# Kernel optimization log

Measured on AMD Instinct MI355X. Metric: run time of the kernel, lower is better.

## Reference

```python
import jax, jax.numpy as jnp
import numpy as np

N_NODES = 50000
N_EDGES = 1600000
N_GRAPHS = 512
IN_DIM = 64
HID = 128
OUT_DIM = 10


def setup_inputs() -> dict:
    key = jax.random.key(0)
    ks = jax.random.split(key, 12)
    x = jax.random.normal(ks[0], (N_NODES, IN_DIM), dtype=jnp.float32)
    edge_index = jax.random.randint(ks[1], (2, N_EDGES), 0, N_NODES, dtype=jnp.int64)
    batch = jnp.sort(jax.random.randint(ks[2], (N_NODES,), 0, N_GRAPHS, dtype=jnp.int64))
    edge_attr = jax.random.uniform(ks[3], (N_EDGES,), dtype=jnp.float32)
    # glorot-ish init for weights
    def lin(k, fan_in, fan_out):
        s = (6.0 / (fan_in + fan_out)) ** 0.5
        return jax.random.uniform(k, (fan_in, fan_out), minval=-s, maxval=s, dtype=jnp.float32)
    return {
        "x": x, "edge_index": edge_index, "batch": batch, "edge_attr": edge_attr,
        "W1": lin(ks[4], IN_DIM, HID), "b1": jnp.zeros((HID,), jnp.float32),
        "W2": lin(ks[5], HID, HID), "b2": jnp.zeros((HID,), jnp.float32),
        "Wm1": lin(ks[6], HID, HID), "bm1": jnp.zeros((HID,), jnp.float32),
        "Wm2": lin(ks[7], HID, OUT_DIM), "bm2": jnp.zeros((OUT_DIM,), jnp.float32),
    }


def _gcn_conv(x, edge_index, edge_weight, W, b, num_nodes):
    """PyG GCNConv: add self-loops, symmetric norm with edge weights, x@W, scatter-add, +bias."""
    loop = jnp.arange(num_nodes, dtype=edge_index.dtype)
    src = jnp.concatenate([edge_index[0], loop])
    dst = jnp.concatenate([edge_index[1], loop])
    ew = jnp.concatenate([edge_weight, jnp.ones((num_nodes,), edge_weight.dtype)])
    deg = jax.ops.segment_sum(ew, dst, num_segments=num_nodes)  # [N]
    dinv = jnp.where(deg > 0, jax.lax.rsqrt(jnp.where(deg > 0, deg, 1.0)), 0.0)
    norm = dinv[src] * ew * dinv[dst]  # [E+N]
    h = x @ W  # [N, F_out]
    msg = h[src] * norm[:, None]  # gather + scale
    out = jax.ops.segment_sum(msg, dst, num_segments=num_nodes)
    return out + b


def reference(x, edge_index, batch, edge_attr, W1, b1, W2, b2, Wm1, bm1, Wm2, bm2):
    n = x.shape[0]
    h = _gcn_conv(x, edge_index, edge_attr, W1, b1, n)
    h = jax.nn.relu(h)  # dropout = identity in eval mode
    h = _gcn_conv(h, edge_index, edge_attr, W2, b2, n)
    h = jax.nn.relu(h)
    pooled = jax.ops.segment_sum(h, batch, num_segments=N_GRAPHS)  # global_add_pool
    z = jax.nn.relu(pooled @ Wm1 + bm1)
    return z @ Wm2 + bm2  # [num_graphs, out_dim]
```

## Files before the change

kernel.cpp:

```cpp
#include <hip/hip_runtime.h>
#include <hip/hip_bf16.h>
#include <hip/hip_fp16.h>
#include <cstdint>

#define HIDC 128
#define FIXSCALE 4194304.0f
#define FIXINV   (1.0f / 4194304.0f)
#define MAXDEG 80

#define BKT_SHIFT 7
#define BKT_NODES 128
#define BKT_CAP   6144
#define BIN_TILE  8192
#define BIN_THREADS 512

typedef _Float16 half8 __attribute__((ext_vector_type(8)));
typedef float float4v __attribute__((ext_vector_type(4)));

__global__ __launch_bounds__(BIN_THREADS) void bin_kernel(
        const int* __restrict__ ei, const float* __restrict__ ea,
        unsigned long long* __restrict__ buck, unsigned int* __restrict__ tails,
        int E, int nbkt) {
    __shared__ unsigned long long rec[BIN_TILE];
    __shared__ unsigned int cnt[BIN_THREADS];
    __shared__ unsigned int startx[BIN_THREADS];
    __shared__ unsigned int cur[BIN_THREADS];
    __shared__ unsigned int gbase[BIN_THREADS];
    int t = threadIdx.x;
    int base = blockIdx.x * BIN_TILE;
    int total = E - base; if (total > BIN_TILE) total = BIN_TILE;

    cnt[t] = 0;
    __syncthreads();

    unsigned int lo[16], dv[16];
#pragma unroll
    for (int j = 0; j < 16; ++j) {
        int e = base + j * BIN_THREADS + t;
        if (e < E) {
            int s = ei[e]; int d = ei[E + e]; float w = ea[e];
            lo[j] = (unsigned int)s |
                    ((unsigned int)__half_as_ushort(__float2half_rn(w)) << 16);
            dv[j] = (unsigned int)d;
            atomicAdd(&cnt[dv[j] >> BKT_SHIFT], 1u);
        } else dv[j] = 0xffffffffu;
    }
    __syncthreads();

    startx[t] = cnt[t];
    __syncthreads();
    for (int off = 1; off < BIN_THREADS; off <<= 1) {
        unsigned int add = (t >= off) ? startx[t - off] : 0u;
        __syncthreads();
        startx[t] += add;
        __syncthreads();
    }
    unsigned int excl = startx[t] - cnt[t];
    startx[t] = excl;
    cur[t] = excl;
    if (t < nbkt) gbase[t] = atomicAdd(&tails[t], cnt[t]);
    __syncthreads();

#pragma unroll
    for (int j = 0; j < 16; ++j) {
        if (dv[j] != 0xffffffffu) {
            unsigned int p = atomicAdd(&cur[dv[j] >> BKT_SHIFT], 1u);
            rec[p] = ((unsigned long long)dv[j] << 32) | (unsigned long long)lo[j];
        }
    }
    __syncthreads();

    for (int i = t; i < total; i += BIN_THREADS) {
        unsigned long long r = rec[i];
        unsigned int b = ((unsigned int)(r >> 32)) >> BKT_SHIFT;
        unsigned int idx = gbase[b] + ((unsigned int)i - startx[b]);
        if (idx < BKT_CAP) buck[(size_t)b * BKT_CAP + idx] = r;
    }
}

__global__ __launch_bounds__(256) void fill_kernel(
        const unsigned long long* __restrict__ buck,
        const unsigned int* __restrict__ tails,
        unsigned long long* __restrict__ degcnt,
        unsigned int* __restrict__ padcsr, int n_nodes) {
    __shared__ unsigned long long deg[BKT_NODES];
    int b = blockIdx.x, t = threadIdx.x;
    if (t < BKT_NODES) deg[t] = 0ull;
    __syncthreads();
    int cnt_b = (int)tails[b]; if (cnt_b > BKT_CAP) cnt_b = BKT_CAP;
    const unsigned long long* rb = buck + (size_t)b * BKT_CAP;
    int nodeBase = b << BKT_SHIFT;
    for (int i = t; i < cnt_b; i += 256) {
        unsigned long long r = rb[i];
        unsigned int lo = (unsigned int)r;
        unsigned int dl = ((unsigned int)(r >> 32)) & (BKT_NODES - 1);
        float w = __half2float(__ushort_as_half((unsigned short)(lo >> 16)));
        unsigned int fx = (unsigned int)(w * FIXSCALE + 0.5f);
        unsigned long long old =
            atomicAdd(&deg[dl], (1ull << 32) | (unsigned long long)fx);
        unsigned int rank = (unsigned int)(old >> 32);
        if (rank < MAXDEG)
            padcsr[(size_t)(nodeBase + dl) * MAXDEG + rank] = lo;
    }
    __syncthreads();
    if (t < BKT_NODES) {
        int node = nodeBase + t;
        if (node < n_nodes) degcnt[node] = deg[t];
    }
}

__global__ void transpose_w2_kernel(const float* __restrict__ W2,
                                    _Float16* __restrict__ W2t) {
    int i = blockIdx.x * 256 + threadIdx.x;
    int k = i >> 7, n = i & 127;
    W2t[n * 128 + k] = (_Float16)W2[i];
}

template <int K>
__global__ __launch_bounds__(256) void gemm_tiled(const float* __restrict__ A,
                                                  const float* __restrict__ W,
                                                  const unsigned long long* __restrict__ degcnt,
                                                  __half* __restrict__ out, int n_nodes) {
    __shared__ float sW[K * 128];
    __shared__ float sX[16 * K];
    int t = threadIdx.x;
    int nodeBase = blockIdx.x * 16;
    for (int i = t; i < K * 128; i += 256) sW[i] = W[i];
    int nAvail = n_nodes - nodeBase; if (nAvail > 16) nAvail = 16;
    for (int i = t; i < nAvail * K; i += 256) sX[i] = A[(size_t)nodeBase * K + i];
    __syncthreads();
    int d = t & 127;
    for (int ni = (t >> 7); ni < nAvail; ni += 2) {
        int node = nodeBase + ni;
        float acc = 0.f;
#pragma unroll
        for (int k = 0; k < K; ++k) acc += sX[ni * K + k] * sW[k * 128 + d];
        unsigned long long v = degcnt[node];
        float di = rsqrtf(1.0f + (float)(unsigned int)(v & 0xffffffffull) * FIXINV);
        out[(size_t)node * 128 + d] = __float2half(acc * di);
    }
}

__global__ __launch_bounds__(256) void gemm2_mfma_kernel(
        const __half* __restrict__ A,
        const _Float16* __restrict__ W2t,
        const unsigned long long* __restrict__ degcnt,
        __half* __restrict__ out, int n_nodes) {
    int wave = threadIdx.x >> 6, lane = threadIdx.x & 63;
    int nodeBase = (blockIdx.x * 4 + wave) * 16;
    if (nodeBase >= n_nodes) return;
    int mrow = lane & 15, quad = lane >> 4;

    int anode = nodeBase + mrow; if (anode >= n_nodes) anode = n_nodes - 1;
    const _Float16* Arow = (const _Float16*)A + (size_t)anode * 128 + quad * 8;
    half8 a[4];
#pragma unroll
    for (int q = 0; q < 4; ++q) a[q] = *(const half8*)(Arow + q * 32);

    float4v acc[8];
#pragma unroll
    for (int nt = 0; nt < 8; ++nt) acc[nt] = (float4v)(0.f);
#pragma unroll
    for (int nt = 0; nt < 8; ++nt) {
        const _Float16* Brow = W2t + (size_t)(nt * 16 + mrow) * 128 + quad * 8;
#pragma unroll
        for (int q = 0; q < 4; ++q) {
            half8 b = *(const half8*)(Brow + q * 32);
            acc[nt] = __builtin_amdgcn_mfma_f32_16x16x32_f16(a[q], b, acc[nt], 0, 0, 0);
        }
    }
#pragma unroll
    for (int r = 0; r < 4; ++r) {
        int node = nodeBase + quad * 4 + r;
        if (node < n_nodes) {
            unsigned long long v = degcnt[node];
            float di = rsqrtf(1.0f + (float)(unsigned int)(v & 0xffffffffull) * FIXINV);
#pragma unroll
            for (int nt = 0; nt < 8; ++nt)
                out[(size_t)node * 128 + nt * 16 + mrow] = __float2half(acc[nt][r] * di);
        }
    }
}

__global__ __launch_bounds__(256) void agg_kernel(const __half* __restrict__ h,
                                                  const unsigned long long* __restrict__ degcnt,
                                                  const unsigned int* __restrict__ padcsr,
                                                  const float* __restrict__ bias,
                                                  __half* __restrict__ out, int n_nodes) {
    int wave = threadIdx.x >> 6;
    int lane = threadIdx.x & 63;
    int node = blockIdx.x * 4 + wave;
    if (node >= n_nodes) return;
    unsigned long long v = degcnt[node];
    int cnt = (int)(v >> 32);
    float di = rsqrtf(1.0f + (float)(unsigned int)(v & 0xffffffffull) * FIXINV);
    const unsigned int* row = padcsr + (size_t)node * MAXDEG;
    float a0 = 0.f, a1 = 0.f;
    int e = 0;
    for (; e + 16 <= cnt; e += 16) {
        unsigned int p[16];
#pragma unroll
        for (int j = 0; j < 16; ++j) p[j] = row[e + j];
        __half2 vv[16];
#pragma unroll
        for (int j = 0; j < 16; ++j)
            vv[j] = *(reinterpret_cast<const __half2*>(h + (size_t)(p[j] & 0xffffu) * HIDC) + lane);
#pragma unroll
        for (int j = 0; j < 16; ++j) {
            float c = __half2float(__ushort_as_half((unsigned short)(p[j] >> 16)));
            float2 f = __half22float2(vv[j]);
            a0 += c * f.x; a1 += c * f.y;
        }
    }
    for (; e + 4 <= cnt; e += 4) {
        unsigned int p[4];
#pragma unroll
        for (int j = 0; j < 4; ++j) p[j] = row[e + j];
        __half2 vv[4];
#pragma unroll
        for (int j = 0; j < 4; ++j)
            vv[j] = *(reinterpret_cast<const __half2*>(h + (size_t)(p[j] & 0xffffu) * HIDC) + lane);
#pragma unroll
        for (int j = 0; j < 4; ++j) {
            float c = __half2float(__ushort_as_half((unsigned short)(p[j] >> 16)));
            float2 f = __half22float2(vv[j]);
            a0 += c * f.x; a1 += c * f.y;
        }
    }
    for (; e < cnt; ++e) {
        unsigned int p = row[e];
        float c = __half2float(__ushort_as_half((unsigned short)(p >> 16)));
        float2 f = __half22float2(*(reinterpret_cast<const __half2*>(h + (size_t)(p & 0xffffu) * HIDC) + lane));
        a0 += c * f.x; a1 += c * f.y;
    }
    float2 fn = __half22float2(*(reinterpret_cast<const __half2*>(h + (size_t)node * HIDC) + lane));
    a0 = di * (a0 + fn.x);
    a1 = di * (a1 + fn.y);
    float2 bb = *(reinterpret_cast<const float2*>(bias) + lane);
    a0 = fmaxf(a0 + bb.x, 0.f);
    a1 = fmaxf(a1 + bb.y, 0.f);
    *(reinterpret_cast<__half2*>(out + (size_t)node * HIDC) + lane) =
        __floats2half2_rn(a0, a1);
}

__global__ __launch_bounds__(128) void pool_mlp_kernel(const __half* __restrict__ h,
                                                       const int* __restrict__ batch,
                                                       const float* __restrict__ Wm1,
                                                       const float* __restrict__ bm1,
                                                       const float* __restrict__ Wm2,
                                                       const float* __restrict__ bm2,
                                                       float* __restrict__ out,
                                                       int n_nodes, int out_dim) {
    int g = blockIdx.x;
    int t = threadIdx.x;
    __shared__ int sb[2];
    if (t < 2) {
        int target = g + t;
        int lo = 0, hi = n_nodes;
        while (lo < hi) { int mid = (lo + hi) >> 1; if (batch[mid] < target) lo = mid + 1; else hi = mid; }
        sb[t] = lo;
    }
    __syncthreads();
    int beg = sb[0], end = sb[1];
    float p = 0.f;
    for (int i = beg; i < end; ++i) p += __half2float(h[(size_t)i * 128 + t]);
    __shared__ float row[128];
    __shared__ float z[128];
    row[t] = p;
    __syncthreads();
    float acc = bm1[t];
#pragma unroll 8
    for (int k = 0; k < 128; ++k) acc += row[k] * Wm1[k * 128 + t];
    z[t] = fmaxf(acc, 0.f);
    __syncthreads();
    if (t < out_dim) {
        float o = bm2[t];
#pragma unroll 8
        for (int k = 0; k < 128; ++k) o += z[k] * Wm2[k * out_dim + t];
        out[g * out_dim + t] = o;
    }
}

extern "C" void kernel_launch(void* const* d_in, const int* in_sizes, int n_in,
                              void* d_out, int out_size, void* d_ws, size_t ws_size,
                              hipStream_t stream) {
    const float* x   = (const float*)d_in[0];
    const int*   ei  = (const int*)d_in[1];
    const int*   bat = (const int*)d_in[2];
    const float* ea  = (const float*)d_in[3];
    const float* W1  = (const float*)d_in[4];
    const float* b1  = (const float*)d_in[5];
    const float* W2  = (const float*)d_in[6];
    const float* b2  = (const float*)d_in[7];
    const float* Wm1 = (const float*)d_in[8];
    const float* bm1 = (const float*)d_in[9];
    const float* Wm2 = (const float*)d_in[10];
    const float* bm2 = (const float*)d_in[11];
    float* out = (float*)d_out;

    const int N = in_sizes[2];
    const int E = in_sizes[1] / 2;
    const int N_GRAPHS = 512;
    const int OUT_DIM = out_size / N_GRAPHS;

    char* ws = (char*)d_ws;
    size_t off = 0;
    auto alloc = [&](size_t bytes) { char* p = ws + off; off += (bytes + 255) & ~size_t(255); return p; };
    __half* bufA    = (__half*)alloc((size_t)N * HIDC * 2);
    __half* bufR    = (__half*)alloc((size_t)N * HIDC * 2);
    unsigned int* padcsr = (unsigned int*)alloc((size_t)N * MAXDEG * 4);
    unsigned long long* degcnt = (unsigned long long*)alloc((size_t)N * 8);
    _Float16* W2t   = (_Float16*)alloc(128 * 128 * 2);
    unsigned int* tails = (unsigned int*)alloc(BIN_THREADS * 4);

    unsigned long long* buck = (unsigned long long*)bufA;
    int nbkt = (N + BKT_NODES - 1) >> BKT_SHIFT;

    hipMemsetAsync(tails, 0, (size_t)nbkt * 4, stream);
    int binBlocks = (E + BIN_TILE - 1) / BIN_TILE;
    bin_kernel<<<binBlocks, BIN_THREADS, 0, stream>>>(ei, ea, buck, tails, E, nbkt);
    fill_kernel<<<nbkt, 256, 0, stream>>>(buck, tails, degcnt, padcsr, N);
    transpose_w2_kernel<<<64, 256, 0, stream>>>(W2, W2t);
    gemm_tiled<64><<<(N + 15) / 16, 256, 0, stream>>>(x, W1, degcnt, bufA, N);
    agg_kernel<<<(N + 3) / 4, 256, 0, stream>>>(bufA, degcnt, padcsr, b1, bufR, N);
    gemm2_mfma_kernel<<<(N + 63) / 64, 256, 0, stream>>>(bufR, W2t, degcnt, bufA, N);
    agg_kernel<<<(N + 3) / 4, 256, 0, stream>>>(bufA, degcnt, padcsr, b2, bufR, N);
    pool_mlp_kernel<<<N_GRAPHS, 128, 0, stream>>>(bufR, bat, Wm1, bm1, Wm2, bm2, out, N, OUT_DIM);
}
```

Before: 309.6 us.

## Use MFMA for first GEMM, merge prep kernels, halve bin tile

Replaces the scalar shared-memory layer-1 GEMM with an MFMA f16 kernel that reads fp32 X, converts it to half and multiplies by a pre-transposed half W1. The W1/W2 transposes and the tails memset are merged into one prep kernel, which removes a memset call and a launch. The bin tile drops to 4096, giving more blocks with fewer registers each. The aggregation loop now uses explicit FMAs, 32-bit index math and clamps the degree to MAXDEG, at the cost of fp16 rounding of X before the matmul.

```diff
diff --git a/kernel.cpp b/kernel.cpp
--- a/kernel.cpp
+++ b/kernel.cpp
@@ -11,11 +11,21 @@
 #define BKT_SHIFT 7
 #define BKT_NODES 128
 #define BKT_CAP   6144
-#define BIN_TILE  8192
+#define BIN_TILE  4096
 #define BIN_THREADS 512
 
 typedef _Float16 half8 __attribute__((ext_vector_type(8)));
 typedef float float4v __attribute__((ext_vector_type(4)));
+
+__global__ __launch_bounds__(256) void prep_kernel(
+        const float* __restrict__ W1, const float* __restrict__ W2,
+        _Float16* __restrict__ W1t, _Float16* __restrict__ W2t,
+        unsigned int* __restrict__ tails, int nbkt) {
+    int i = blockIdx.x * 256 + threadIdx.x;
+    if (i < 16384) { int k = i >> 7, n = i & 127; W2t[n * 128 + k] = (_Float16)W2[i]; }
+    if (i < 8192)  { int k = i >> 7, n = i & 127; W1t[n * 64 + k]  = (_Float16)W1[i]; }
+    if (i < nbkt) tails[i] = 0u;
+}
 
 __global__ __launch_bounds__(BIN_THREADS) void bin_kernel(
         const int* __restrict__ ei, const float* __restrict__ ea,
@@ -33,9 +43,9 @@
     cnt[t] = 0;
     __syncthreads();
 
-    unsigned int lo[16], dv[16];
-#pragma unroll
-    for (int j = 0; j < 16; ++j) {
+    unsigned int lo[8], dv[8];
+#pragma unroll
+    for (int j = 0; j < 8; ++j) {
         int e = base + j * BIN_THREADS + t;
         if (e < E) {
             int s = ei[e]; int d = ei[E + e]; float w = ea[e];
@@ -62,7 +72,7 @@
     __syncthreads();
 
 #pragma unroll
-    for (int j = 0; j < 16; ++j) {
+    for (int j = 0; j < 8; ++j) {
         if (dv[j] != 0xffffffffu) {
             unsigned int p = atomicAdd(&cur[dv[j] >> BKT_SHIFT], 1u);
             rec[p] = ((unsigned long long)dv[j] << 32) | (unsigned long long)lo[j];
@@ -109,35 +119,51 @@
     }
 }
 
-__global__ void transpose_w2_kernel(const float* __restrict__ W2,
-                                    _Float16* __restrict__ W2t) {
-    int i = blockIdx.x * 256 + threadIdx.x;
-    int k = i >> 7, n = i & 127;
-    W2t[n * 128 + k] = (_Float16)W2[i];
-}
-
-template <int K>
-__global__ __launch_bounds__(256) void gemm_tiled(const float* __restrict__ A,
-                                                  const float* __restrict__ W,
-                                                  const unsigned long long* __restrict__ degcnt,
-                                                  __half* __restrict__ out, int n_nodes) {
-    __shared__ float sW[K * 128];
-    __shared__ float sX[16 * K];
-    int t = threadIdx.x;
-    int nodeBase = blockIdx.x * 16;
-    for (int i = t; i < K * 128; i += 256) sW[i] = W[i];
-    int nAvail = n_nodes - nodeBase; if (nAvail > 16) nAvail = 16;
-    for (int i = t; i < nAvail * K; i += 256) sX[i] = A[(size_t)nodeBase * K + i];
-    __syncthreads();
-    int d = t & 127;
-    for (int ni = (t >> 7); ni < nAvail; ni += 2) {
-        int node = nodeBase + ni;
-        float acc = 0.f;
-#pragma unroll
-        for (int k = 0; k < K; ++k) acc += sX[ni * K + k] * sW[k * 128 + d];
-        unsigned long long v = degcnt[node];
-        float di = rsqrtf(1.0f + (float)(unsigned int)(v & 0xffffffffull) * FIXINV);
-        out[(size_t)node * 128 + d] = __float2half(acc * di);
+__global__ __launch_bounds__(256) void gemm1_mfma_kernel(
+        const float* __restrict__ X,
+        const _Float16* __restrict__ W1t,
+        const unsigned long long* __restrict__ degcnt,
+        __half* __restrict__ out, int n_nodes) {
+    int wave = threadIdx.x >> 6, lane = threadIdx.x & 63;
+    int nodeBase = (blockIdx.x * 4 + wave) * 16;
+    if (nodeBase >= n_nodes) return;
+    int mrow = lane & 15, quad = lane >> 4;
+
+    int anode = nodeBase + mrow; if (anode >= n_nodes) anode = n_nodes - 1;
+    const float* Arow = X + (size_t)anode * 64 + quad * 8;
+    half8 a[2];
+#pragma unroll
+    for (int q = 0; q < 2; ++q) {
+        float4v f0 = *(const float4v*)(Arow + q * 32);
+        float4v f1 = *(const float4v*)(Arow + q * 32 + 4);
+        half8 hv;
+#pragma unroll
+        for (int j = 0; j < 4; ++j) { hv[j] = (_Float16)f0[j]; hv[j + 4] = (_Float16)f1[j]; }
+        a[q] = hv;
+    }
+
+    float4v acc[8];
+#pragma unroll
+    for (int nt = 0; nt < 8; ++nt) acc[nt] = (float4v)(0.f);
+#pragma unroll
+    for (int nt = 0; nt < 8; ++nt) {
+        const _Float16* Brow = W1t + (size_t)(nt * 16 + mrow) * 64 + quad * 8;
+#pragma unroll
+        for (int q = 0; q < 2; ++q) {
+            half8 b = *(const half8*)(Brow + q * 32);
+            acc[nt] = __builtin_amdgcn_mfma_f32_16x16x32_f16(a[q], b, acc[nt], 0, 0, 0);
+        }
+    }
+#pragma unroll
+    for (int r = 0; r < 4; ++r) {
+        int node = nodeBase + quad * 4 + r;
+        if (node < n_nodes) {
+            unsigned long long v = degcnt[node];
+            float di = rsqrtf(1.0f + (float)(unsigned int)(v & 0xffffffffull) * FIXINV);
+#pragma unroll
+            for (int nt = 0; nt < 8; ++nt)
+                out[(size_t)node * 128 + nt * 16 + mrow] = __float2half(acc[nt][r] * di);
+        }
     }
 }
 
@@ -193,6 +219,7 @@
     if (node >= n_nodes) return;
     unsigned long long v = degcnt[node];
     int cnt = (int)(v >> 32);
+    if (cnt > MAXDEG) cnt = MAXDEG;
     float di = rsqrtf(1.0f + (float)(unsigned int)(v & 0xffffffffull) * FIXINV);
     const unsigned int* row = padcsr + (size_t)node * MAXDEG;
     float a0 = 0.f, a1 = 0.f;
@@ -204,12 +231,12 @@
         __half2 vv[16];
 #pragma unroll
         for (int j = 0; j < 16; ++j)
-            vv[j] = *(reinterpret_cast<const __half2*>(h + (size_t)(p[j] & 0xffffu) * HIDC) + lane);
+            vv[j] = *(reinterpret_cast<const __half2*>(h + (p[j] & 0xffffu) * HIDC) + lane);
 #pragma unroll
         for (int j = 0; j < 16; ++j) {
             float c = __half2float(__ushort_as_half((unsigned short)(p[j] >> 16)));
             float2 f = __half22float2(vv[j]);
-            a0 += c * f.x; a1 += c * f.y;
+            a0 = fmaf(c, f.x, a0); a1 = fmaf(c, f.y, a1);
         }
     }
     for (; e + 4 <= cnt; e += 4) {
@@ -219,19 +246,19 @@
         __half2 vv[4];
 #pragma unroll
         for (int j = 0; j < 4; ++j)
-            vv[j] = *(reinterpret_cast<const __half2*>(h + (size_t)(p[j] & 0xffffu) * HIDC) + lane);
+            vv[j] = *(reinterpret_cast<const __half2*>(h + (p[j] & 0xffffu) * HIDC) + lane);
 #pragma unroll
         for (int j = 0; j < 4; ++j) {
             float c = __half2float(__ushort_as_half((unsigned short)(p[j] >> 16)));
             float2 f = __half22float2(vv[j]);
-            a0 += c * f.x; a1 += c * f.y;
+            a0 = fmaf(c, f.x, a0); a1 = fmaf(c, f.y, a1);
         }
     }
     for (; e < cnt; ++e) {
         unsigned int p = row[e];
         float c = __half2float(__ushort_as_half((unsigned short)(p >> 16)));
-        float2 f = __half22float2(*(reinterpret_cast<const __half2*>(h + (size_t)(p & 0xffffu) * HIDC) + lane));
-        a0 += c * f.x; a1 += c * f.y;
+        float2 f = __half22float2(*(reinterpret_cast<const __half2*>(h + (p & 0xffffu) * HIDC) + lane));
+        a0 = fmaf(c, f.x, a0); a1 = fmaf(c, f.y, a1);
     }
     float2 fn = __half22float2(*(reinterpret_cast<const __half2*>(h + (size_t)node * HIDC) + lane));
     a0 = di * (a0 + fn.x);
@@ -311,17 +338,17 @@
     unsigned int* padcsr = (unsigned int*)alloc((size_t)N * MAXDEG * 4);
     unsigned long long* degcnt = (unsigned long long*)alloc((size_t)N * 8);
     _Float16* W2t   = (_Float16*)alloc(128 * 128 * 2);
+    _Float16* W1t   = (_Float16*)alloc(128 * 64 * 2);
     unsigned int* tails = (unsigned int*)alloc(BIN_THREADS * 4);
 
     unsigned long long* buck = (unsigned long long*)bufA;
     int nbkt = (N + BKT_NODES - 1) >> BKT_SHIFT;
 
-    hipMemsetAsync(tails, 0, (size_t)nbkt * 4, stream);
+    prep_kernel<<<64, 256, 0, stream>>>(W1, W2, W1t, W2t, tails, nbkt);
     int binBlocks = (E + BIN_TILE - 1) / BIN_TILE;
     bin_kernel<<<binBlocks, BIN_THREADS, 0, stream>>>(ei, ea, buck, tails, E, nbkt);
     fill_kernel<<<nbkt, 256, 0, stream>>>(buck, tails, degcnt, padcsr, N);
-    transpose_w2_kernel<<<64, 256, 0, stream>>>(W2, W2t);
-    gemm_tiled<64><<<(N + 15) / 16, 256, 0, stream>>>(x, W1, degcnt, bufA, N);
+    gemm1_mfma_kernel<<<(N + 63) / 64, 256, 0, stream>>>(x, W1t, degcnt, bufA, N);
     agg_kernel<<<(N + 3) / 4, 256, 0, stream>>>(bufA, degcnt, padcsr, b1, bufR, N);
     gemm2_mfma_kernel<<<(N + 63) / 64, 256, 0, stream>>>(bufR, W2t, degcnt, bufA, N);
     agg_kernel<<<(N + 3) / 4, 256, 0, stream>>>(bufA, degcnt, padcsr, b2, bufR, N);
```

Result: faster. 303.4 us (-2.0%).
